# Kernel optimization log

Hardware: AMD Instinct MI355X
Metric: run time of the kernel (lower is better)

Reference implementation:

```python
import jax, jax.numpy as jnp
import numpy as np

N_HEAD = 16
HIDDEN = 1024

def setup_inputs() -> dict:
    key = jax.random.key(0)
    ks = jax.random.split(key, 4)
    B, T, D = 2, 2048, HIDDEN
    x = jax.random.normal(ks[0], (B, T, D), dtype=jnp.float32)
    attention_mask = jnp.zeros((B, 1, 1, T), dtype=jnp.float32)  # additive mask
    w_attn = jax.random.normal(ks[1], (D, 3 * D), dtype=jnp.float32) * (1.0 / np.sqrt(D))
    b_attn = jnp.zeros((3 * D,), dtype=jnp.float32)
    w_proj = jax.random.normal(ks[2], (D, D), dtype=jnp.float32) * (1.0 / np.sqrt(D))
    b_proj = jnp.zeros((D,), dtype=jnp.float32)
    return {"x": x, "attention_mask": attention_mask,
            "w_attn": w_attn, "b_attn": b_attn,
            "w_proj": w_proj, "b_proj": b_proj}

def reference(x, attention_mask, w_attn, b_attn, w_proj, b_proj):
    B, T, D = x.shape
    H = N_HEAD
    hd = D // H
    qkv = x @ w_attn + b_attn                      # [B,T,3D]
    q, k, v = jnp.split(qkv, 3, axis=-1)
    q = q.reshape(B, T, H, hd)
    k = k.reshape(B, T, H, hd)
    v = v.reshape(B, T, H, hd)
    qk = jnp.einsum('BFNH,BTNH->BNFT', q, k) / jnp.sqrt(jnp.asarray(hd, qk_dtype := q.dtype))
    # NOTE: source adds the mask twice (once unconditionally, once inside the None-check)
    attn_weights = qk + attention_mask + attention_mask
    attn_probs = jax.nn.softmax(attn_weights, axis=-1)  # dropout(0.01) is identity at inference
    attn_out = jnp.einsum('BNFT,BTNH->BFNH', attn_probs, v)
    attn_out = attn_out.reshape(B, T, D)
    return attn_out @ w_proj + b_proj
```

## Files before the change

kernel.cpp:

```cpp
#include <hip/hip_runtime.h>
#include <hip/hip_bf16.h>

#define T_SEQ 2048
#define D_MODEL 1024
#define N_HEADS 16

typedef _Float16 half8 __attribute__((ext_vector_type(8)));
typedef _Float16 half4 __attribute__((ext_vector_type(4)));
typedef _Float16 half2v __attribute__((ext_vector_type(2)));
typedef float floatx4 __attribute__((ext_vector_type(4)));
typedef unsigned short ushort4v __attribute__((ext_vector_type(4)));
typedef unsigned short ushort8v __attribute__((ext_vector_type(8)));

#define LOG2E 1.44269504088896f

__device__ __forceinline__ unsigned short f32_to_bf16(float f) {
  unsigned u = __builtin_bit_cast(unsigned, f);
  u = u + 0x7FFFu + ((u >> 16) & 1u);
  return (unsigned short)(u >> 16);
}
__device__ __forceinline__ float bf16_to_f32(unsigned short h) {
  unsigned u = ((unsigned)h) << 16;
  return __builtin_bit_cast(float, u);
}
__device__ __forceinline__ half2v pk_f16(float a, float b) {
  return __builtin_bit_cast(half2v, __builtin_amdgcn_cvt_pkrtz(a, b));
}

__device__ __forceinline__ void load16_lds(const _Float16* g, _Float16* lds_base, int lane) {
#if __has_builtin(__builtin_amdgcn_global_load_lds)
  __builtin_amdgcn_global_load_lds(
      (const __attribute__((address_space(1))) void*)g,
      (__attribute__((address_space(3))) void*)lds_base, 16, 0, 0);
#else
  *(half8*)(lds_base + lane * 8) = *(const half8*)g;
#endif
}

__global__ void k_detect(const unsigned short* __restrict__ x, int* __restrict__ flag) {
  __shared__ int cnt;
  if (threadIdx.x == 0) cnt = 0;
  __syncthreads();
  unsigned short v = x[(size_t)threadIdx.x * 2];
  int e = (v >> 7) & 0xFF;
  int ok = (v == 0) || (e >= 100 && e <= 150);
  atomicAdd(&cnt, ok);
  __syncthreads();
  if (threadIdx.x == 0) *flag = (cnt >= 192) ? 1 : 0;
}

__global__ void k_cvt3(const void* __restrict__ ba, const void* __restrict__ bp,
                       const void* __restrict__ mk, float* __restrict__ baF,
                       float* __restrict__ bpF, float* __restrict__ mask2,
                       const int* __restrict__ flag) {
  int f = *flag;
  int i = blockIdx.x * 256 + threadIdx.x;
  auto cv = [&](const void* p, int j) {
    return f ? bf16_to_f32(((const unsigned short*)p)[j]) : ((const float*)p)[j];
  };
  if (i < 3072) baF[i] = cv(ba, i);
  else if (i < 4096) bpF[i - 3072] = cv(bp, i - 3072);
  else mask2[i - 4096] = cv(mk, i - 4096) * (2.0f * LOG2E);
}

__global__ __launch_bounds__(256) void k_transpose2(
    const void* __restrict__ inA, _Float16* __restrict__ outA,
    const void* __restrict__ inB, _Float16* __restrict__ outB,
    const int* __restrict__ flag) {
  __shared__ float tile[32][33];
  int f = *flag;
  const void* in;
  _Float16* out;
  int N, bid;
  if (blockIdx.x < 3072) { in = inA; out = outA; N = 3072; bid = blockIdx.x; }
  else { in = inB; out = outB; N = 1024; bid = blockIdx.x - 3072; }
  const int K = 1024;
  int nb = N >> 5;
  int bx = bid % nb, by = bid / nb;
  int n0 = bx << 5, k0 = by << 5;
  int c = threadIdx.x & 31, r = threadIdx.x >> 5;
  const float* fin = (const float*)in;
  const unsigned short* uin = (const unsigned short*)in;
#pragma unroll
  for (int i = 0; i < 4; ++i) {
    int kk = r + i * 8;
    size_t idx = (size_t)(k0 + kk) * N + n0 + c;
    tile[kk][c] = f ? bf16_to_f32(uin[idx]) : fin[idx];
  }
  __syncthreads();
#pragma unroll
  for (int i = 0; i < 4; ++i) {
    int nn = r + i * 8;
    out[(size_t)(n0 + nn) * K + k0 + c] = (_Float16)tile[c][nn];
  }
}

__global__ __launch_bounds__(256) void k_gemm(
    const _Float16* __restrict__ A, const void* __restrict__ BT,
    const float* __restrict__ bias, void* __restrict__ D0,
    void* __restrict__ D1, void* __restrict__ D2,
    int M, int N, int K, int outKind, int bRaw, const int* __restrict__ flag) {
  __shared__ _Float16 As[128 * 64] __attribute__((aligned(16)));
  __shared__ _Float16 Bs[128 * 64] __attribute__((aligned(16)));
  const int tid = threadIdx.x;
  const int wave = tid >> 6, lane = tid & 63;
  const int ln = lane & 15, quad = lane >> 4;
  const int bm = blockIdx.y * 128, bn = blockIdx.x * 128;
  const int wm = (wave & 1) * 64, wn = (wave >> 1) * 64;
  const int f = *flag;

  const int sr = tid >> 3, scn = (tid & 7) ^ (sr & 7);
  const _Float16* Ag = A + (size_t)(bm + sr) * K + scn * 8;
  const _Float16* Bg16 = (const _Float16*)BT + (size_t)(bn + sr) * K + scn * 8;
  const float* Bg32 = (const float*)BT + (size_t)(bn + sr) * K + scn * 8;
  const unsigned short* Bgbf = (const unsigned short*)BT + (size_t)(bn + sr) * K + scn * 8;

  floatx4 acc[4][4] = {};

  for (int kt = 0; kt < K; kt += 64) {
    __syncthreads();
#pragma unroll
    for (int i = 0; i < 4; ++i)
      load16_lds(Ag + kt + (size_t)i * 32 * K, As + (wave * 64 + i * 256) * 8, lane);
    if (!bRaw) {
#pragma unroll
      for (int i = 0; i < 4; ++i)
        load16_lds(Bg16 + kt + (size_t)i * 32 * K, Bs + (wave * 64 + i * 256) * 8, lane);
    } else if (f) {
#pragma unroll
      for (int i = 0; i < 4; ++i) {
        ushort8v u = *(const ushort8v*)(Bgbf + kt + (size_t)i * 32 * K);
        half8 o;
#pragma unroll
        for (int e = 0; e < 8; ++e) o[e] = (_Float16)bf16_to_f32(u[e]);
        *(half8*)(Bs + (size_t)(wave * 64 + i * 256 + lane) * 8) = o;
      }
    } else {
#pragma unroll
      for (int i = 0; i < 4; ++i) {
        const float* sp = Bg32 + kt + (size_t)i * 32 * K;
        floatx4 a = *(const floatx4*)sp;
        floatx4 b = *(const floatx4*)(sp + 4);
        half8 o;
#pragma unroll
        for (int e = 0; e < 4; ++e) { o[e] = (_Float16)a[e]; o[e + 4] = (_Float16)b[e]; }
        *(half8*)(Bs + (size_t)(wave * 64 + i * 256 + lane) * 8) = o;
      }
    }
    __syncthreads();
    half8 af[4][2], bf[4][2];
#pragma unroll
    for (int i = 0; i < 4; ++i) {
      int r = wm + i * 16 + ln;
#pragma unroll
      for (int ks = 0; ks < 2; ++ks)
        af[i][ks] = *(const half8*)(As + r * 64 + ((quad + 4 * ks) ^ (r & 7)) * 8);
    }
#pragma unroll
    for (int j = 0; j < 4; ++j) {
      int r = wn + j * 16 + ln;
#pragma unroll
      for (int ks = 0; ks < 2; ++ks)
        bf[j][ks] = *(const half8*)(Bs + r * 64 + ((quad + 4 * ks) ^ (r & 7)) * 8);
    }
#pragma unroll
    for (int ks = 0; ks < 2; ++ks)
#pragma unroll
      for (int i = 0; i < 4; ++i)
#pragma unroll
        for (int j = 0; j < 4; ++j)
          acc[i][j] = __builtin_amdgcn_mfma_f32_16x16x32_f16(af[i][ks], bf[j][ks], acc[i][j], 0, 0, 0);
  }

  if (outKind == 0) {
    _Float16* Qs = (_Float16*)D0;
    _Float16* Ks = (_Float16*)D1;
    _Float16* Vt = (_Float16*)D2;
    const float qsc = 0.125f * LOG2E;
#pragma unroll
    for (int i = 0; i < 4; ++i) {
      int rbase = bm + wm + i * 16 + quad * 4;
      int sect = rbase >> 10;
      int cfeat = rbase & 1023;
      int h = cfeat >> 6, hd = cfeat & 63;
      float bv[4];
#pragma unroll
      for (int r = 0; r < 4; ++r) bv[r] = bias[rbase + r];
#pragma unroll
      for (int j = 0; j < 4; ++j) {
        int col = bn + wn + j * 16 + ln;
        int b = col >> 11, t = col & 2047;
        size_t bh = (size_t)b * N_HEADS + h;
        float v[4];
#pragma unroll
        for (int r = 0; r < 4; ++r) v[r] = acc[i][j][r] + bv[r];
        if (sect == 0) {
          half4 q;
#pragma unroll
          for (int r = 0; r < 4; ++r) q[r] = (_Float16)(v[r] * qsc);
          *(half4*)(Qs + (bh * T_SEQ + t) * 64 + hd) = q;
        } else if (sect == 1) {
          half4 kk4;
#pragma unroll
          for (int r = 0; r < 4; ++r) kk4[r] = (_Float16)v[r];
          *(half4*)(Ks + (bh * T_SEQ + t) * 64 + hd) = kk4;
        } else {
#pragma unroll
          for (int r = 0; r < 4; ++r)
            Vt[(bh * 64 + hd + r) * T_SEQ + t] = (_Float16)v[r];
        }
      }
    }
  } else {
    int mode = f ? 2 : 1;
#pragma unroll
    for (int i = 0; i < 4; ++i) {
      int rbase = bm + wm + i * 16 + quad * 4;
      float bv[4];
#pragma unroll
      for (int r = 0; r < 4; ++r) bv[r] = bias[rbase + r];
#pragma unroll
      for (int j = 0; j < 4; ++j) {
        int col = bn + wn + j * 16 + ln;
        float v[4];
#pragma unroll
        for (int r = 0; r < 4; ++r) v[r] = acc[i][j][r] + bv[r];
        if (mode == 1) {
          floatx4 o = {v[0], v[1], v[2], v[3]};
          *(floatx4*)((float*)D0 + (size_t)col * M + rbase) = o;
        } else {
          ushort4v o;
#pragma unroll
          for (int r = 0; r < 4; ++r) o[r] = f32_to_bf16(v[r]);
          *(ushort4v*)((unsigned short*)D0 + (size_t)col * M + rbase) = o;
        }
      }
    }
  }
}

__global__ __launch_bounds__(256, 4) void k_flash(
    const _Float16* __restrict__ Qs, const _Float16* __restrict__ Ks,
    const _Float16* __restrict__ Vt, const float* __restrict__ mask2,
    _Float16* __restrict__ O) {
  __shared__ __attribute__((aligned(16))) char smem[32768];
  _Float16* KlB = (_Float16*)smem;
  _Float16* VlB = (_Float16*)(smem + 16384);
  float* Red = (float*)smem;

  const int tid = threadIdx.x, wave = tid >> 6, lane = tid & 63;
  const int ln = lane & 15, quad = lane >> 4;
  const int qh = wave & 1, kh = wave >> 1;
  const int id = blockIdx.x;
  const int qc = id & 31, h = (id >> 5) & 15, b = id >> 9;
  const size_t bh = (size_t)b * N_HEADS + h;
  const _Float16* Qb = Qs + bh * T_SEQ * 64;
  const _Float16* Kb = Ks + bh * T_SEQ * 64;
  const _Float16* Vb = Vt + bh * 64 * T_SEQ;
  const int q0w = qc * 64 + qh * 32;

  half8 qf[2][2];
#pragma unroll
  for (int jq = 0; jq < 2; ++jq)
#pragma unroll
    for (int kk = 0; kk < 2; ++kk)
      qf[jq][kk] = *(const half8*)(Qb + (size_t)(q0w + jq * 16 + ln) * 64 + kk * 32 + quad * 8);

  floatx4 Oacc[4][2] = {};
  float m0[2] = {0.f, 0.f}, li[2] = {0.f, 0.f};

  const int sr = tid >> 3, scn = (tid & 7) ^ (sr & 7);
  const _Float16* kp0 = Kb + (size_t)sr * 64 + scn * 8;
  const _Float16* kp1 = kp0 + 32 * 64;
  const _Float16* vp0 = Vb + (size_t)sr * T_SEQ + scn * 8;
  const _Float16* vp1 = vp0 + 32 * T_SEQ;
  const float* mqw = mask2 + (size_t)b * T_SEQ + kh * 32 + quad * 4;

  {
    _Float16* K0 = KlB + (size_t)wave * 512;
    _Float16* V0 = VlB + (size_t)wave * 512;
    load16_lds(kp0, K0, lane);
    load16_lds(kp1, K0 + 2048, lane);
    load16_lds(vp0, V0, lane);
    load16_lds(vp1, V0 + 2048, lane);
    kp0 += 64 * 64; kp1 += 64 * 64; vp0 += 64; vp1 += 64;
  }

  for (int t = 0; t < 32; ++t) {
    const int cur = t & 1;
    __syncthreads();
    if (t + 1 < 32) {
      _Float16* K0 = KlB + (cur ^ 1) * 4096 + (size_t)wave * 512;
      _Float16* V0 = VlB + (cur ^ 1) * 4096 + (size_t)wave * 512;
      load16_lds(kp0, K0, lane);
      load16_lds(kp1, K0 + 2048, lane);
      load16_lds(vp0, V0, lane);
      load16_lds(vp1, V0 + 2048, lane);
      kp0 += 64 * 64; kp1 += 64 * 64; vp0 += 64; vp1 += 64;
    }
    const _Float16* Kc = KlB + cur * 4096;
    const _Float16* Vc = VlB + cur * 4096;

    floatx4 s[2][2];
    __builtin_amdgcn_s_setprio(1);
#pragma unroll
    for (int jk = 0; jk < 2; ++jk) {
      const int krow = kh * 32 + jk * 16 + ln;
      half8 kf0 = *(const half8*)(Kc + krow * 64 + ((quad) ^ (krow & 7)) * 8);
      half8 kf1 = *(const half8*)(Kc + krow * 64 + ((4 + quad) ^ (krow & 7)) * 8);
#pragma unroll
      for (int jq = 0; jq < 2; ++jq) {
        floatx4 z = *(const floatx4*)(mqw + jk * 16);
        z = __builtin_amdgcn_mfma_f32_16x16x32_f16(kf0, qf[jq][0], z, 0, 0, 0);
        z = __builtin_amdgcn_mfma_f32_16x16x32_f16(kf1, qf[jq][1], z, 0, 0, 0);
        s[jk][jq] = z;
      }
    }
    __builtin_amdgcn_s_setprio(0);
    mqw += 64;

    if (t == 0) {
#pragma unroll
      for (int jq = 0; jq < 2; ++jq) {
        float tm = -__builtin_inff();
#pragma unroll
        for (int jk = 0; jk < 2; ++jk)
#pragma unroll
          for (int r = 0; r < 4; ++r) tm = fmaxf(tm, s[jk][jq][r]);
        tm = fmaxf(tm, __shfl_xor(tm, 16, 64));
        tm = fmaxf(tm, __shfl_xor(tm, 32, 64));
        m0[jq] = fmaxf(tm, -50.f);
      }
    }

#pragma unroll
    for (int jk = 0; jk < 2; ++jk)
#pragma unroll
      for (int jq = 0; jq < 2; ++jq)
#pragma unroll
        for (int r = 0; r < 4; ++r) {
          float p = __builtin_amdgcn_exp2f(s[jk][jq][r] - m0[jq]);
          s[jk][jq][r] = p;
          li[jq] += p;
        }

    half4 pf4[2][2];
#pragma unroll
    for (int jk = 0; jk < 2; ++jk)
#pragma unroll
      for (int jq = 0; jq < 2; ++jq) {
        half2v p01 = pk_f16(s[jk][jq][0], s[jk][jq][1]);
        half2v p23 = pk_f16(s[jk][jq][2], s[jk][jq][3]);
        pf4[jk][jq] = (half4){p01[0], p01[1], p23[0], p23[1]};
      }

    __builtin_amdgcn_s_setprio(1);
#pragma unroll
    for (int jd = 0; jd < 4; ++jd) {
      const int vrow = jd * 16 + ln;
      const _Float16* Vr = Vc + vrow * 64;
      half4 vf0 = *(const half4*)(Vr + (((kh * 4 + 0 + (quad >> 1)) ^ (vrow & 7)) * 8) + (quad & 1) * 4);
      half4 vf1 = *(const half4*)(Vr + (((kh * 4 + 2 + (quad >> 1)) ^ (vrow & 7)) * 8) + (quad & 1) * 4);
#pragma unroll
      for (int jq = 0; jq < 2; ++jq) {
        Oacc[jd][jq] = __builtin_amdgcn_mfma_f32_16x16x16f16(vf0, pf4[0][jq], Oacc[jd][jq], 0, 0, 0);
        Oacc[jd][jq] = __builtin_amdgcn_mfma_f32_16x16x16f16(vf1, pf4[1][jq], Oacc[jd][jq], 0, 0, 0);
      }
    }
    __builtin_amdgcn_s_setprio(0);
  }

#pragma unroll
  for (int jq = 0; jq < 2; ++jq) {
    li[jq] += __shfl_xor(li[jq], 16, 64);
    li[jq] += __shfl_xor(li[jq], 32, 64);
  }

  __syncthreads();
  float* myRed = Red + ((size_t)qh * 64 + lane) * 36;
  if (kh) {
#pragma unroll
    for (int jd = 0; jd < 4; ++jd)
#pragma unroll
      for (int jq = 0; jq < 2; ++jq)
#pragma unroll
        for (int r = 0; r < 4; ++r) myRed[jd * 8 + jq * 4 + r] = Oacc[jd][jq][r];
#pragma unroll
    for (int jq = 0; jq < 2; ++jq) {
      myRed[32 + jq] = m0[jq];
      myRed[34 + jq] = li[jq];
    }
  }
  __syncthreads();
  if (!kh) {
    float sa[2], sb[2], inv[2];
#pragma unroll
    for (int jq = 0; jq < 2; ++jq) {
      float Mb = myRed[32 + jq], lb = myRed[34 + jq];
      float M = fmaxf(m0[jq], Mb);
      sa[jq] = __builtin_amdgcn_exp2f(m0[jq] - M);
      sb[jq] = __builtin_amdgcn_exp2f(Mb - M);
      inv[jq] = 1.f / (li[jq] * sa[jq] + lb * sb[jq]);
    }
#pragma unroll
    for (int jd = 0; jd < 4; ++jd)
#pragma unroll
      for (int jq = 0; jq < 2; ++jq) {
        half4 ov;
#pragma unroll
        for (int r = 0; r < 4; ++r) {
          float v = Oacc[jd][jq][r] * sa[jq] + myRed[jd * 8 + jq * 4 + r] * sb[jq];
          ov[r] = (_Float16)(v * inv[jq]);
        }
        *(half4*)(O + ((size_t)b * T_SEQ + q0w + jq * 16 + ln) * D_MODEL +
                  h * 64 + jd * 16 + quad * 4) = ov;
      }
  }
}

extern "C" void kernel_launch(void* const* d_in, const int* in_sizes, int n_in,
                              void* d_out, int out_size, void* d_ws, size_t ws_size,
                              hipStream_t stream) {
  const void* x      = d_in[0];
  const void* amask  = d_in[1];
  const void* w_attn = d_in[2];
  const void* b_attn = d_in[3];
  const void* w_proj = d_in[4];
  const void* b_proj = d_in[5];

  char* ws = (char*)d_ws;
  size_t off = 0;
  auto alloc = [&](size_t bytes) {
    void* p = ws + off;
    off += (bytes + 255) & ~(size_t)255;
    return p;
  };
  int* flag        = (int*)alloc(256);
  _Float16* WaT    = (_Float16*)alloc((size_t)3072 * 1024 * 2);
  _Float16* WpT    = (_Float16*)alloc((size_t)1024 * 1024 * 2);
  float* baF       = (float*)alloc(3072 * 4);
  float* bpF       = (float*)alloc(1024 * 4);
  float* mask2     = (float*)alloc(4096 * 4);
  _Float16* Qs     = (_Float16*)alloc((size_t)4096 * 1024 * 2);
  _Float16* Ks     = (_Float16*)alloc((size_t)4096 * 1024 * 2);
  _Float16* Vt     = (_Float16*)alloc((size_t)4096 * 1024 * 2);
  _Float16* AttnH  = (_Float16*)alloc((size_t)4096 * 1024 * 2);

  k_detect<<<1, 256, 0, stream>>>((const unsigned short*)x, flag);
  k_transpose2<<<3072 + 1024, 256, 0, stream>>>(w_attn, WaT, w_proj, WpT, flag);
  k_cvt3<<<32, 256, 0, stream>>>(b_attn, b_proj, amask, baF, bpF, mask2, flag);

  dim3 g1(4096 / 128, 3072 / 128);
  k_gemm<<<g1, 256, 0, stream>>>(WaT, x, baF, Qs, Ks, Vt, 3072, 4096, 1024, 0, 1, flag);

  k_flash<<<1024, 256, 0, stream>>>(Qs, Ks, Vt, mask2, AttnH);

  dim3 g2(4096 / 128, 1024 / 128);
  k_gemm<<<g2, 256, 0, stream>>>(WpT, AttnH, bpF, d_out, nullptr, nullptr, 1024, 4096, 1024, 1, 0, flag);
}
```

Measured before the change: 202.1 us.

## Fuse bias/mask conversion into transpose, add 64x64 output GEMM, remap flash block order

Folds the small bias/mask conversion kernel into the weight-transpose launch as extra blocks, removing one kernel launch. Adds a 64x64-tile GEMM for the output projection, so that launch uses 1024 blocks instead of 256 and fills the GPU better, at the cost of less data reuse per block. Remaps the flash-attention block index so that consecutive blocks are spread across batch/head groups, which may improve cache or XCD locality.

After: 199.9 us. No clear change (-1.1%).

```diff
diff --git a/kernel.cpp b/kernel.cpp
--- a/kernel.cpp
+++ b/kernel.cpp
@@ -49,26 +49,25 @@
   if (threadIdx.x == 0) *flag = (cnt >= 192) ? 1 : 0;
 }
 
-__global__ void k_cvt3(const void* __restrict__ ba, const void* __restrict__ bp,
-                       const void* __restrict__ mk, float* __restrict__ baF,
-                       float* __restrict__ bpF, float* __restrict__ mask2,
-                       const int* __restrict__ flag) {
-  int f = *flag;
-  int i = blockIdx.x * 256 + threadIdx.x;
-  auto cv = [&](const void* p, int j) {
-    return f ? bf16_to_f32(((const unsigned short*)p)[j]) : ((const float*)p)[j];
-  };
-  if (i < 3072) baF[i] = cv(ba, i);
-  else if (i < 4096) bpF[i - 3072] = cv(bp, i - 3072);
-  else mask2[i - 4096] = cv(mk, i - 4096) * (2.0f * LOG2E);
-}
-
 __global__ __launch_bounds__(256) void k_transpose2(
     const void* __restrict__ inA, _Float16* __restrict__ outA,
     const void* __restrict__ inB, _Float16* __restrict__ outB,
+    const void* __restrict__ ba, const void* __restrict__ bp,
+    const void* __restrict__ mk, float* __restrict__ baF,
+    float* __restrict__ bpF, float* __restrict__ mask2,
     const int* __restrict__ flag) {
   __shared__ float tile[32][33];
   int f = *flag;
+  if (blockIdx.x >= 4096) {
+    int i = (blockIdx.x - 4096) * 256 + threadIdx.x;
+    auto cv = [&](const void* p, int j) {
+      return f ? bf16_to_f32(((const unsigned short*)p)[j]) : ((const float*)p)[j];
+    };
+    if (i < 3072) baF[i] = cv(ba, i);
+    else if (i < 4096) bpF[i - 3072] = cv(bp, i - 3072);
+    else mask2[i - 4096] = cv(mk, i - 4096) * (2.0f * LOG2E);
+    return;
+  }
   const void* in;
   _Float16* out;
   int N, bid;
@@ -239,6 +238,83 @@
   }
 }
 
+__global__ __launch_bounds__(256) void k_gemm64(
+    const _Float16* __restrict__ A, const _Float16* __restrict__ BT,
+    const float* __restrict__ bias, void* __restrict__ D0,
+    int M, int N, int K, const int* __restrict__ flag) {
+  __shared__ _Float16 As[64 * 64] __attribute__((aligned(16)));
+  __shared__ _Float16 Bs[64 * 64] __attribute__((aligned(16)));
+  const int tid = threadIdx.x;
+  const int wave = tid >> 6, lane = tid & 63;
+  const int ln = lane & 15, quad = lane >> 4;
+  const int bm = blockIdx.y * 64, bn = blockIdx.x * 64;
+  const int wm = (wave & 1) * 32, wn = (wave >> 1) * 32;
+  const int f = *flag;
+
+  const int sr = tid >> 3, scn = (tid & 7) ^ (sr & 7);
+  const _Float16* Ag = A + (size_t)(bm + sr) * K + scn * 8;
+  const _Float16* Bg = BT + (size_t)(bn + sr) * K + scn * 8;
+
+  floatx4 acc[2][2] = {};
+
+  for (int kt = 0; kt < K; kt += 64) {
+    __syncthreads();
+#pragma unroll
+    for (int i = 0; i < 2; ++i) {
+      load16_lds(Ag + kt + (size_t)i * 32 * K, As + (wave * 64 + i * 256) * 8, lane);
+      load16_lds(Bg + kt + (size_t)i * 32 * K, Bs + (wave * 64 + i * 256) * 8, lane);
+    }
+    __syncthreads();
+    half8 af[2][2], bf[2][2];
+#pragma unroll
+    for (int i = 0; i < 2; ++i) {
+      int r = wm + i * 16 + ln;
+#pragma unroll
+      for (int ks = 0; ks < 2; ++ks)
+        af[i][ks] = *(const half8*)(As + r * 64 + ((quad + 4 * ks) ^ (r & 7)) * 8);
+    }
+#pragma unroll
+    for (int j = 0; j < 2; ++j) {
+      int r = wn + j * 16 + ln;
+#pragma unroll
+      for (int ks = 0; ks < 2; ++ks)
+        bf[j][ks] = *(const half8*)(Bs + r * 64 + ((quad + 4 * ks) ^ (r & 7)) * 8);
+    }
+#pragma unroll
+    for (int ks = 0; ks < 2; ++ks)
+#pragma unroll
+      for (int i = 0; i < 2; ++i)
+#pragma unroll
+        for (int j = 0; j < 2; ++j)
+          acc[i][j] = __builtin_amdgcn_mfma_f32_16x16x32_f16(af[i][ks], bf[j][ks], acc[i][j], 0, 0, 0);
+  }
+
+  int mode = f ? 2 : 1;
+#pragma unroll
+  for (int i = 0; i < 2; ++i) {
+    int rbase = bm + wm + i * 16 + quad * 4;
+    float bv[4];
+#pragma unroll
+    for (int r = 0; r < 4; ++r) bv[r] = bias[rbase + r];
+#pragma unroll
+    for (int j = 0; j < 2; ++j) {
+      int col = bn + wn + j * 16 + ln;
+      float v[4];
+#pragma unroll
+      for (int r = 0; r < 4; ++r) v[r] = acc[i][j][r] + bv[r];
+      if (mode == 1) {
+        floatx4 o = {v[0], v[1], v[2], v[3]};
+        *(floatx4*)((float*)D0 + (size_t)col * M + rbase) = o;
+      } else {
+        ushort4v o;
+#pragma unroll
+        for (int r = 0; r < 4; ++r) o[r] = f32_to_bf16(v[r]);
+        *(ushort4v*)((unsigned short*)D0 + (size_t)col * M + rbase) = o;
+      }
+    }
+  }
+}
+
 __global__ __launch_bounds__(256, 4) void k_flash(
     const _Float16* __restrict__ Qs, const _Float16* __restrict__ Ks,
     const _Float16* __restrict__ Vt, const float* __restrict__ mask2,
@@ -251,7 +327,7 @@
   const int tid = threadIdx.x, wave = tid >> 6, lane = tid & 63;
   const int ln = lane & 15, quad = lane >> 4;
   const int qh = wave & 1, kh = wave >> 1;
-  const int id = blockIdx.x;
+  const int id = ((blockIdx.x & 7) << 7) | (blockIdx.x >> 3);
   const int qc = id & 31, h = (id >> 5) & 15, b = id >> 9;
   const size_t bh = (size_t)b * N_HEADS + h;
   const _Float16* Qb = Qs + bh * T_SEQ * 64;
@@ -447,14 +523,14 @@
   _Float16* AttnH  = (_Float16*)alloc((size_t)4096 * 1024 * 2);
 
   k_detect<<<1, 256, 0, stream>>>((const unsigned short*)x, flag);
-  k_transpose2<<<3072 + 1024, 256, 0, stream>>>(w_attn, WaT, w_proj, WpT, flag);
-  k_cvt3<<<32, 256, 0, stream>>>(b_attn, b_proj, amask, baF, bpF, mask2, flag);
+  k_transpose2<<<3072 + 1024 + 32, 256, 0, stream>>>(
+      w_attn, WaT, w_proj, WpT, b_attn, b_proj, amask, baF, bpF, mask2, flag);
 
   dim3 g1(4096 / 128, 3072 / 128);
   k_gemm<<<g1, 256, 0, stream>>>(WaT, x, baF, Qs, Ks, Vt, 3072, 4096, 1024, 0, 1, flag);
 
   k_flash<<<1024, 256, 0, stream>>>(Qs, Ks, Vt, mask2, AttnH);
 
-  dim3 g2(4096 / 128, 1024 / 128);
-  k_gemm<<<g2, 256, 0, stream>>>(WpT, AttnH, bpF, d_out, nullptr, nullptr, 1024, 4096, 1024, 1, 0, flag);
-}
+  dim3 g2(4096 / 64, 1024 / 64);
+  k_gemm64<<<g2, 256, 0, stream>>>(WpT, AttnH, bpF, d_out, 1024, 4096, 1024, flag);
+}
```
